# Kernel tuning notes

Hardware: AMD Instinct MI355X
Metric: run time of the kernel (lower is better)

Reference implementation:

```python
import jax, jax.numpy as jnp
import numpy as np

R_FRAC = 0.5  # r_token


def setup_inputs() -> dict:
    key = jax.random.key(0)
    B, T, C = 64, 577, 1024
    hidden_states = jax.random.normal(key, (B, T, C), dtype=jnp.float32)
    return {"hidden_states": hidden_states}


def _match_indices(x, r):
    # Bipartite soft matching (class_token=True, distill_token=False).
    metric = x / jnp.linalg.norm(x, axis=-1, keepdims=True)
    a, b = metric[:, ::2, :], metric[:, 1::2, :]  # [B, Ta, C], [B, Tb, C]
    scores = jnp.einsum('bic,bjc->bij', a, b)     # [B, Ta, Tb]
    scores = scores.at[:, 0, :].set(-jnp.inf)     # protect CLS token (even index 0)
    node_max = scores.max(axis=-1)                # best sim of each src to any dst
    node_idx = scores.argmax(axis=-1)             # matched dst for each src
    edge_idx = jnp.argsort(-node_max, axis=-1)    # descending by similarity
    unm_idx = jnp.sort(edge_idx[:, r:], axis=-1)  # unmerged src (sorted: keeps CLS first)
    src_idx = edge_idx[:, :r]                     # src tokens to merge
    dst_idx = jnp.take_along_axis(node_idx, src_idx, axis=-1)
    return unm_idx, src_idx, dst_idx


def _merge_sum(v, unm_idx, src_idx, dst_idx):
    # Gather unmerged + scatter-add merged src into dst, then concat.
    src, dst = v[:, ::2, :], v[:, 1::2, :]
    unm = jnp.take_along_axis(src, unm_idx[..., None], axis=1)
    srcg = jnp.take_along_axis(src, src_idx[..., None], axis=1)
    dst = jax.vmap(lambda d, i, s: d.at[i].add(s))(dst, dst_idx, srcg)
    return jnp.concatenate([unm, dst], axis=1)


def reference(hidden_states):
    x = hidden_states
    B, T, C = x.shape
    protected = 1  # class token
    r = min(int(R_FRAC * T), (T - protected) // 2)  # 288 for T=577
    unm_idx, src_idx, dst_idx = _match_indices(x, r)
    # merge_wavg with size=None -> size = ones
    size = jnp.ones((B, T, 1), dtype=x.dtype)
    xm = _merge_sum(x * size, unm_idx, src_idx, dst_idx)
    sm = _merge_sum(size, unm_idx, src_idx, dst_idx)
    return xm / sm  # [B, T - r, C]
```

## Files before the change

### kernel.cpp

```cpp
#include <hip/hip_runtime.h>
#include <math.h>


#define B_   64
#define T_   577
#define C_   1024
#define NA   289
#define NB   288
#define EPS_MARGIN 0.01f

#define RPAD 384
#define EXTRA_CAP 12

typedef __bf16 bf16x8 __attribute__((ext_vector_type(8)));
typedef float  floatx4 __attribute__((ext_vector_type(4)));
typedef unsigned long long u64;

#define ECNT_OFF   0
#define GRPWIN_OFF 98304
#define EXTRA_OFF  (GRPWIN_OFF + 1179648)
#define DST_OFF    (EXTRA_OFF + 2359296)

__device__ __forceinline__ u64 shfl_xor_u64(u64 v, int msk) {
  unsigned int lo = (unsigned int)v, hi = (unsigned int)(v >> 32);
  lo = __shfl_xor(lo, msk, 64);
  hi = __shfl_xor(hi, msk, 64);
  return ((u64)hi << 32) | (u64)lo;
}
__device__ __forceinline__ double shfl_xor_f64(double v, int msk) {
  u64 u = __double_as_longlong(v);
  return __longlong_as_double((long long)shfl_xor_u64(u, msk));
}

__device__ __forceinline__ unsigned int fkey(float s) {
  unsigned int fb = __float_as_uint(s);
  return (fb & 0x80000000u) ? ~fb : (fb | 0x80000000u);
}
__device__ __forceinline__ float keyf(unsigned int k) {
  return (k & 0x80000000u) ? __uint_as_float(k ^ 0x80000000u) : __uint_as_float(~k);
}
__device__ __forceinline__ u64 packsc(float s, int col) {
  return ((u64)fkey(s) << 32) | (u64)(0xFFFFFFFFu - (unsigned int)col);
}
__device__ __forceinline__ int pcol(u64 p) {
  return (int)(0xFFFFFFFFu - (unsigned int)(p & 0xFFFFFFFFull));
}
__device__ __forceinline__ float pscore(u64 p) { return keyf((unsigned int)(p >> 32)); }

__device__ __forceinline__ unsigned int pk_bf16_trunc(unsigned int e1, unsigned int e0) {
  return __builtin_amdgcn_perm(e1, e0, 0x07060302u);
}

__device__ __forceinline__ void load16f(const float* x, size_t off, float* v) {
  const float4* p = (const float4*)(x + off);
  float4 a = p[0], b = p[1], c = p[2], d = p[3];
  v[0]=a.x; v[1]=a.y; v[2]=a.z; v[3]=a.w;
  v[4]=b.x; v[5]=b.y; v[6]=b.z; v[7]=b.w;
  v[8]=c.x; v[9]=c.y; v[10]=c.z; v[11]=c.w;
  v[12]=d.x; v[13]=d.y; v[14]=d.z; v[15]=d.w;
}

__global__ __launch_bounds__(256) void k_prep(const float* __restrict__ x,
                                              unsigned int* __restrict__ y) {
  int wv = threadIdx.x >> 6, lane = threadIdx.x & 63;
  int token = blockIdx.x * 4 + wv;
  int t = token % T_;
  int r8 = (t >> 1) & 7;

  float v[16];
  load16f(x, (size_t)token * C_ + lane * 16, v);
  float ss = 0.f;
#pragma unroll
  for (int i = 0; i < 16; ++i) ss += v[i] * v[i];
#pragma unroll
  for (int d = 1; d < 64; d <<= 1) ss += __shfl_xor(ss, d, 64);
  float rn = rsqrtf(ss);
#pragma unroll
  for (int i = 0; i < 16; ++i) v[i] *= rn;

  uint4 g0, g1;
  g0.x = pk_bf16_trunc(__float_as_uint(v[1]),  __float_as_uint(v[0]));
  g0.y = pk_bf16_trunc(__float_as_uint(v[3]),  __float_as_uint(v[2]));
  g0.z = pk_bf16_trunc(__float_as_uint(v[5]),  __float_as_uint(v[4]));
  g0.w = pk_bf16_trunc(__float_as_uint(v[7]),  __float_as_uint(v[6]));
  g1.x = pk_bf16_trunc(__float_as_uint(v[9]),  __float_as_uint(v[8]));
  g1.y = pk_bf16_trunc(__float_as_uint(v[11]), __float_as_uint(v[10]));
  g1.z = pk_bf16_trunc(__float_as_uint(v[13]), __float_as_uint(v[12]));
  g1.w = pk_bf16_trunc(__float_as_uint(v[15]), __float_as_uint(v[14]));

  int ga = 2 * lane, gb = 2 * lane + 1;
  int da = (ga & ~7) | ((ga & 7) ^ r8);
  int db = (gb & ~7) | ((gb & 7) ^ r8);
  uint4* yb = (uint4*)((char*)y + (size_t)token * 2048);
  yb[da] = g0;
  yb[db] = g1;
}


#define GLOADLDS16(GP, LP)                                                    \
  __builtin_amdgcn_global_load_lds(                                           \
      (const __attribute__((address_space(1))) void*)(GP),                    \
      (__attribute__((address_space(3))) void*)(LP), 16, 0, 0)

#define STAGE(CUR, KC) do {                                                   \
  _Pragma("unroll")                                                           \
  for (int e_ = 0; e_ < 6; ++e_)                                              \
    GLOADLDS16(src[e_] + (KC) * 128, smem[CUR] + ldsoff[e_]);                 \
} while (0)

#define MFMAC(BUFP) do {                                                      \
  const unsigned char* buf_ = (BUFP);                                         \
  _Pragma("unroll")                                                           \
  for (int s_ = 0; s_ < 2; ++s_) {                                            \
    int slot_ = (s_ * 4 + q) ^ sw;                                            \
    bf16x8 af_[3], bg_[3];                                                    \
    _Pragma("unroll")                                                         \
    for (int ii_ = 0; ii_ < 3; ++ii_)                                         \
      af_[ii_] = *(const bf16x8*)(buf_ + ((ib + ii_) * 16 + m) * 128 + slot_ * 16); \
    _Pragma("unroll")                                                         \
    for (int jj_ = 0; jj_ < 3; ++jj_)                                         \
      bg_[jj_] = *(const bf16x8*)(buf_ + 12288 + ((jb + jj_) * 16 + m) * 128 + slot_ * 16); \
    _Pragma("unroll")                                                         \
    for (int ii_ = 0; ii_ < 3; ++ii_)                                         \
      _Pragma("unroll")                                                       \
      for (int jj_ = 0; jj_ < 3; ++jj_)                                       \
        acc[ii_][jj_] = __builtin_amdgcn_mfma_f32_16x16x32_bf16(af_[ii_], bg_[jj_], acc[ii_][jj_], 0, 0, 0); \
  }                                                                           \
} while (0)

__global__ __launch_bounds__(256, 2) void k_scores(const unsigned int* __restrict__ y,
                                                   u64* __restrict__ grpwin,
                                                   unsigned int* __restrict__ ecnt,
                                                   u64* __restrict__ extras) {
  __shared__ unsigned char smem[2][24576];
  int tid = threadIdx.x;
  int b  = blockIdx.x;
  int rt = blockIdx.y;
  int ct = blockIdx.z;
  int wv = tid >> 6, lane = tid & 63;
  int m = lane & 15, q = lane >> 4;
  int sw = m & 7;

  const char* src[6];
  int ldsoff[6];
#pragma unroll
  for (int e = 0; e < 6; ++e) {
    int L = ((wv * 6 + e) * 64 + lane) * 16;
    int row = L >> 7;
    int sl  = (L >> 4) & 7;
    int isB = row >= 96;
    int r2  = isB ? row - 96 : row;
    int tok;
    if (isB) tok = 2 * (ct * 96 + r2) + 1;
    else { tok = 2 * (rt * 96 + r2); if (tok > 576) tok = 576; }
    src[e] = (const char*)y + (size_t)(b * T_ + tok) * 2048 + sl * 16;
    ldsoff[e] = (wv * 6 + e) * 1024;
  }

  floatx4 acc[3][3];
#pragma unroll
  for (int ii = 0; ii < 3; ++ii)
#pragma unroll
    for (int jj = 0; jj < 3; ++jj) acc[ii][jj] = (floatx4){0, 0, 0, 0};

  const int ib = (wv >> 1) * 3;
  const int jb = (wv & 1) * 3;

  STAGE(0, 0);
  __syncthreads();
  int cur = 0;
  for (int kc = 0; kc < 15; ++kc) {
    STAGE(cur ^ 1, kc + 1);
    MFMAC(smem[cur]);
    __syncthreads();
    cur ^= 1;
  }
  MFMAC(smem[cur]);

  int g = ct * 2 + (wv & 1);
#pragma unroll
  for (int ii = 0; ii < 3; ++ii) {
#pragma unroll
    for (int r = 0; r < 4; ++r) {
      u64 pj[3];
#pragma unroll
      for (int jj = 0; jj < 3; ++jj) {
        float s = acc[ii][jj][r];
        pj[jj] = packsc(s, ct * 96 + (jb + jj) * 16 + m);
      }
      u64 pk = pj[0];
      if (pj[1] > pk) pk = pj[1];
      if (pj[2] > pk) pk = pj[2];
#pragma unroll
      for (int d = 1; d < 16; d <<= 1) {
        u64 o = shfl_xor_u64(pk, d);
        if (o > pk) pk = o;
      }
      int grow = rt * 96 + (ib + ii) * 16 + q * 4 + r;
      float thr = pscore(pk) - EPS_MARGIN;
      size_t rbase = (size_t)b * RPAD + grow;
#pragma unroll
      for (int jj = 0; jj < 3; ++jj) {
        if (pj[jj] != pk && pscore(pj[jj]) >= thr) {
          unsigned int idx = atomicAdd(&ecnt[rbase], 1u);
          if (idx < EXTRA_CAP) extras[rbase * EXTRA_CAP + idx] = pj[jj];
        }
      }
      if (m == 0) grpwin[rbase * 6 + g] = pk;
    }
  }
}

__global__ __launch_bounds__(256) void k_recheck(const float* __restrict__ x,
                                                 const u64* __restrict__ grpwin,
                                                 const unsigned int* __restrict__ ecnt,
                                                 const u64* __restrict__ extras,
                                                 int* __restrict__ dst) {
  int wid = threadIdx.x >> 6, lane = threadIdx.x & 63;
  int gw = blockIdx.x * 4 + wid;
  int b = gw / NB, i = gw - b * NB + 1;
  size_t rbase = (size_t)b * RPAD + i;

  u64 v = (lane < 6) ? grpwin[rbase * 6 + lane] : 0ull;
#pragma unroll
  for (int d = 1; d < 8; d <<= 1) {
    u64 o = shfl_xor_u64(v, d);
    if (o > v) v = o;
  }
  {
    unsigned int lo = (unsigned int)v, hi = (unsigned int)(v >> 32);
    lo = __shfl(lo, 0, 64); hi = __shfl(hi, 0, 64);
    v = ((u64)hi << 32) | lo;
  }
  float thr = pscore(v) - EPS_MARGIN;

  u64 cand[14]; int nc = 0;
#pragma unroll
  for (int t = 0; t < 6; ++t) {
    u64 w = grpwin[rbase * 6 + t];
    if (pscore(w) >= thr && nc < 14) cand[nc++] = w;
  }
  unsigned int ec = ecnt[rbase]; if (ec > EXTRA_CAP) ec = EXTRA_CAP;
  for (unsigned int t = 0; t < ec; ++t) {
    u64 w = extras[rbase * EXTRA_CAP + t];
    if (pscore(w) >= thr && nc < 14) cand[nc++] = w;
  }

  int best;
  if (nc <= 1) {
    best = pcol(v);
  } else {
    float av[16];
    load16f(x, (size_t)(b * T_ + 2 * i) * C_ + lane * 16, av);
    double bs = -1e300; int bc = 1 << 30;
    for (int c = 0; c < nc; ++c) {
      int col = pcol(cand[c]);
      float bv[16];
      load16f(x, (size_t)(b * T_ + 2 * col + 1) * C_ + lane * 16, bv);
      double dot = 0.0, nsq = 0.0;
#pragma unroll
      for (int t = 0; t < 16; ++t) {
        dot += (double)av[t] * (double)bv[t];
        nsq += (double)bv[t] * (double)bv[t];
      }
#pragma unroll
      for (int d = 32; d >= 1; d >>= 1) {
        dot += shfl_xor_f64(dot, d);
        nsq += shfl_xor_f64(nsq, d);
      }
      double s = dot / sqrt(nsq);
      if (s > bs || (s == bs && col < bc)) { bs = s; bc = col; }
    }
    best = bc;
  }
  if (lane == 0) dst[b * NA + i] = best;
}

__global__ __launch_bounds__(256) void k_merge(const float* __restrict__ x,
                                               const int* __restrict__ dst,
                                               float* __restrict__ out) {
  __shared__ int dstv[NA];
  __shared__ unsigned short lists[4][292];
  __shared__ int cnts[4];
  int b = blockIdx.y, tid = threadIdx.x;
  int orow_base = blockIdx.x * 4;

  for (int i = tid; i < NA; i += 256) dstv[i] = (i >= 1) ? dst[b * NA + i] : -1;
  if (tid < 4) cnts[tid] = 0;
  __syncthreads();

  for (int i = 1 + tid; i <= 288; i += 256) {
    int d = dstv[i];
#pragma unroll
    for (int w4 = 0; w4 < 4; ++w4) {
      int orow_w = orow_base + w4;
      if (orow_w >= 1 && orow_w < NA && d == orow_w - 1) {
        int idx = atomicAdd(&cnts[w4], 1);
        lists[w4][idx] = (unsigned short)i;
      }
    }
  }
  __syncthreads();

  int wv = tid >> 6, lane = tid & 63;
  int orow = orow_base + wv;
  if (orow >= NA) return;

  const size_t xb = (size_t)b * T_ * C_;
  int c0 = lane * 16;
  float acc[16];
  float inv = 1.0f;

  if (orow == 0) {
    load16f(x, xb + c0, acc);
  } else {
    int j = orow - 1;
    load16f(x, xb + (size_t)(2 * j + 1) * C_ + c0, acc);
    int cnt = cnts[wv];
    for (int e = 0; e < cnt; ++e) {
      int i = lists[wv][e];
      float tv[16];
      load16f(x, xb + (size_t)(2 * i) * C_ + c0, tv);
#pragma unroll
      for (int t = 0; t < 16; ++t) acc[t] += tv[t];
    }
    inv = 1.0f / (float)(cnt + 1);
  }

  float4* op = (float4*)(out + ((size_t)b * NA + orow) * C_ + c0);
  op[0] = make_float4(acc[0]*inv,  acc[1]*inv,  acc[2]*inv,  acc[3]*inv);
  op[1] = make_float4(acc[4]*inv,  acc[5]*inv,  acc[6]*inv,  acc[7]*inv);
  op[2] = make_float4(acc[8]*inv,  acc[9]*inv,  acc[10]*inv, acc[11]*inv);
  op[3] = make_float4(acc[12]*inv, acc[13]*inv, acc[14]*inv, acc[15]*inv);
}

extern "C" void kernel_launch(void* const* d_in, const int* in_sizes, int n_in,
                              void* d_out, int out_size, void* d_ws, size_t ws_size,
                              hipStream_t stream) {
  const float* x = (const float*)d_in[0];
  float* out     = (float*)d_out;
  char* ws = (char*)d_ws;
  unsigned int* ecnt = (unsigned int*)(ws + ECNT_OFF);
  u64* grpwin        = (u64*)(ws + GRPWIN_OFF);
  u64* extras        = (u64*)(ws + EXTRA_OFF);
  int* dst           = (int*)(ws + DST_OFF);

  unsigned int* y = (unsigned int*)d_out;

  hipMemsetAsync(ecnt, 0, (size_t)B_ * RPAD * sizeof(unsigned int), stream);
  k_prep   <<<(B_ * T_) / 4, 256, 0, stream>>>(x, y);
  k_scores <<<dim3(B_, 4, 3), 256, 0, stream>>>(y, grpwin, ecnt, extras);
  k_recheck<<<B_ * NB / 4, 256, 0, stream>>>(x, grpwin, ecnt, extras, dst);
  k_merge  <<<dim3((NA + 3) / 4, B_), 256, 0, stream>>>(x, dst, out);
}
```

Measured before the change: 345.5 us.

## Fuse score GEMM, argmax and recheck into one per-row-tile kernel

The separate scores and recheck kernels, the memset and the global workspace for group winners and extras are replaced by one kernel. Each block computes a 32-row by 288-column score tile in LDS, takes the row max with a wave reduction, and rechecks near-ties in fp64 against the original fp32 inputs. This removes two launches, a memset and global round-trips of candidate data. In exchange, A rows are staged per 32-row tile while the full B set is reloaded by each of the 9 row tiles. The tie margin is also tightened, so fewer rows fall into the slow fp64 recheck path.

```diff
diff --git a/kernel.cpp b/kernel.cpp
--- a/kernel.cpp
+++ b/kernel.cpp
@@ -7,19 +7,13 @@
 #define C_   1024
 #define NA   289
 #define NB   288
-#define EPS_MARGIN 0.01f
-
-#define RPAD 384
-#define EXTRA_CAP 12
+#define EPS_MARGIN 0.0025f
 
 typedef __bf16 bf16x8 __attribute__((ext_vector_type(8)));
 typedef float  floatx4 __attribute__((ext_vector_type(4)));
 typedef unsigned long long u64;
 
-#define ECNT_OFF   0
-#define GRPWIN_OFF 98304
-#define EXTRA_OFF  (GRPWIN_OFF + 1179648)
-#define DST_OFF    (EXTRA_OFF + 2359296)
+#define DST_OFF 0
 
 __device__ __forceinline__ u64 shfl_xor_u64(u64 v, int msk) {
   unsigned int lo = (unsigned int)v, hi = (unsigned int)(v >> 32);
@@ -59,6 +53,11 @@
   v[8]=c.x; v[9]=c.y; v[10]=c.z; v[11]=c.w;
   v[12]=d.x; v[13]=d.y; v[14]=d.z; v[15]=d.w;
 }
+
+#define GLOADLDS16(GP, LP)                                                    \
+  __builtin_amdgcn_global_load_lds(                                           \
+      (const __attribute__((address_space(1))) void*)(GP),                    \
+      (__attribute__((address_space(3))) void*)(LP), 16, 0, 0)
 
 __global__ __launch_bounds__(256) void k_prep(const float* __restrict__ x,
                                               unsigned int* __restrict__ y) {
@@ -97,183 +96,157 @@
 }
 
 
-#define GLOADLDS16(GP, LP)                                                    \
-  __builtin_amdgcn_global_load_lds(                                           \
-      (const __attribute__((address_space(1))) void*)(GP),                    \
-      (__attribute__((address_space(3))) void*)(LP), 16, 0, 0)
-
-#define STAGE(CUR, KC) do {                                                   \
+#define STAGE2(CUR, KC) do {                                                  \
   _Pragma("unroll")                                                           \
-  for (int e_ = 0; e_ < 6; ++e_)                                              \
+  for (int e_ = 0; e_ < 10; ++e_)                                             \
     GLOADLDS16(src[e_] + (KC) * 128, smem[CUR] + ldsoff[e_]);                 \
 } while (0)
 
-#define MFMAC(BUFP) do {                                                      \
+#define MFMAC2(BUFP) do {                                                     \
   const unsigned char* buf_ = (BUFP);                                         \
   _Pragma("unroll")                                                           \
   for (int s_ = 0; s_ < 2; ++s_) {                                            \
     int slot_ = (s_ * 4 + q) ^ sw;                                            \
-    bf16x8 af_[3], bg_[3];                                                    \
+    bf16x8 af_, bg_[9];                                                       \
+    af_ = *(const bf16x8*)(buf_ + (rfrag * 16 + m) * 128 + slot_ * 16);       \
     _Pragma("unroll")                                                         \
-    for (int ii_ = 0; ii_ < 3; ++ii_)                                         \
-      af_[ii_] = *(const bf16x8*)(buf_ + ((ib + ii_) * 16 + m) * 128 + slot_ * 16); \
+    for (int jj_ = 0; jj_ < 9; ++jj_)                                         \
+      bg_[jj_] = *(const bf16x8*)(buf_ + 4096 + ((cbase + jj_ * 16) + m) * 128 + slot_ * 16); \
     _Pragma("unroll")                                                         \
-    for (int jj_ = 0; jj_ < 3; ++jj_)                                         \
-      bg_[jj_] = *(const bf16x8*)(buf_ + 12288 + ((jb + jj_) * 16 + m) * 128 + slot_ * 16); \
-    _Pragma("unroll")                                                         \
-    for (int ii_ = 0; ii_ < 3; ++ii_)                                         \
-      _Pragma("unroll")                                                       \
-      for (int jj_ = 0; jj_ < 3; ++jj_)                                       \
-        acc[ii_][jj_] = __builtin_amdgcn_mfma_f32_16x16x32_bf16(af_[ii_], bg_[jj_], acc[ii_][jj_], 0, 0, 0); \
+    for (int jj_ = 0; jj_ < 9; ++jj_)                                         \
+      acc[jj_] = __builtin_amdgcn_mfma_f32_16x16x32_bf16(af_, bg_[jj_], acc[jj_], 0, 0, 0); \
   }                                                                           \
 } while (0)
 
-__global__ __launch_bounds__(256, 2) void k_scores(const unsigned int* __restrict__ y,
-                                                   u64* __restrict__ grpwin,
-                                                   unsigned int* __restrict__ ecnt,
-                                                   u64* __restrict__ extras) {
-  __shared__ unsigned char smem[2][24576];
+__global__ __launch_bounds__(256, 2) void k_spick(const unsigned int* __restrict__ y,
+                                                  const float* __restrict__ x,
+                                                  int* __restrict__ dst) {
+  __shared__ unsigned char smem[2][40960];
   int tid = threadIdx.x;
   int b  = blockIdx.x;
   int rt = blockIdx.y;
-  int ct = blockIdx.z;
   int wv = tid >> 6, lane = tid & 63;
   int m = lane & 15, q = lane >> 4;
   int sw = m & 7;
 
-  const char* src[6];
-  int ldsoff[6];
-#pragma unroll
-  for (int e = 0; e < 6; ++e) {
-    int L = ((wv * 6 + e) * 64 + lane) * 16;
+  const char* src[10];
+  int ldsoff[10];
+#pragma unroll
+  for (int e = 0; e < 10; ++e) {
+    int u = wv * 10 + e;
+    int L = u * 1024 + lane * 16;
     int row = L >> 7;
-    int sl  = (L >> 4) & 7;
-    int isB = row >= 96;
-    int r2  = isB ? row - 96 : row;
-    int tok;
-    if (isB) tok = 2 * (ct * 96 + r2) + 1;
-    else { tok = 2 * (rt * 96 + r2); if (tok > 576) tok = 576; }
-    src[e] = (const char*)y + (size_t)(b * T_ + tok) * 2048 + sl * 16;
-    ldsoff[e] = (wv * 6 + e) * 1024;
-  }
-
-  floatx4 acc[3][3];
-#pragma unroll
-  for (int ii = 0; ii < 3; ++ii)
-#pragma unroll
-    for (int jj = 0; jj < 3; ++jj) acc[ii][jj] = (floatx4){0, 0, 0, 0};
-
-  const int ib = (wv >> 1) * 3;
-  const int jb = (wv & 1) * 3;
-
-  STAGE(0, 0);
+    int s  = (L >> 4) & 7;
+    int tok, fslot;
+    if (row < 32) {
+      int l8 = row & 7;
+      int i = rt * 32 + 1 + row;
+      tok = 2 * i;
+      fslot = s ^ l8 ^ ((row + 1) & 7);
+    } else {
+      int j = row - 32;
+      tok = 2 * j + 1;
+      fslot = s;
+    }
+    src[e] = (const char*)y + (size_t)(b * T_ + tok) * 2048 + fslot * 16;
+    ldsoff[e] = u * 1024;
+  }
+
+  floatx4 acc[9];
+#pragma unroll
+  for (int jj = 0; jj < 9; ++jj) acc[jj] = (floatx4){0, 0, 0, 0};
+
+  const int rfrag = wv & 1;
+  const int cbase = (wv >> 1) * 144;
+
+  STAGE2(0, 0);
   __syncthreads();
   int cur = 0;
   for (int kc = 0; kc < 15; ++kc) {
-    STAGE(cur ^ 1, kc + 1);
-    MFMAC(smem[cur]);
+    STAGE2(cur ^ 1, kc + 1);
+    MFMAC2(smem[cur]);
     __syncthreads();
     cur ^= 1;
   }
-  MFMAC(smem[cur]);
-
-  int g = ct * 2 + (wv & 1);
-#pragma unroll
-  for (int ii = 0; ii < 3; ++ii) {
+  MFMAC2(smem[cur]);
+
+  float* sc = (float*)smem[0];
+#pragma unroll
+  for (int jj = 0; jj < 9; ++jj) {
 #pragma unroll
     for (int r = 0; r < 4; ++r) {
-      u64 pj[3];
-#pragma unroll
-      for (int jj = 0; jj < 3; ++jj) {
-        float s = acc[ii][jj][r];
-        pj[jj] = packsc(s, ct * 96 + (jb + jj) * 16 + m);
-      }
-      u64 pk = pj[0];
-      if (pj[1] > pk) pk = pj[1];
-      if (pj[2] > pk) pk = pj[2];
-#pragma unroll
-      for (int d = 1; d < 16; d <<= 1) {
-        u64 o = shfl_xor_u64(pk, d);
-        if (o > pk) pk = o;
-      }
-      int grow = rt * 96 + (ib + ii) * 16 + q * 4 + r;
-      float thr = pscore(pk) - EPS_MARGIN;
-      size_t rbase = (size_t)b * RPAD + grow;
-#pragma unroll
-      for (int jj = 0; jj < 3; ++jj) {
-        if (pj[jj] != pk && pscore(pj[jj]) >= thr) {
-          unsigned int idx = atomicAdd(&ecnt[rbase], 1u);
-          if (idx < EXTRA_CAP) extras[rbase * EXTRA_CAP + idx] = pj[jj];
+      int srow = rfrag * 16 + q * 4 + r;
+      int scol = cbase + jj * 16 + m;
+      sc[srow * 288 + scol] = acc[jj][r];
+    }
+  }
+  __syncthreads();
+
+  for (int rr = 0; rr < 8; ++rr) {
+    int lrow = wv * 8 + rr;
+    int i = rt * 32 + 1 + lrow;
+
+    u64 ps[5]; u64 pk = 0;
+#pragma unroll
+    for (int s5 = 0; s5 < 5; ++s5) {
+      int col = s5 * 64 + lane;
+      ps[s5] = (col < 288) ? packsc(sc[lrow * 288 + col], col) : 0ull;
+      if (ps[s5] > pk) pk = ps[s5];
+    }
+#pragma unroll
+    for (int d = 1; d < 64; d <<= 1) {
+      u64 o = shfl_xor_u64(pk, d);
+      if (o > pk) pk = o;
+    }
+    float thr = pscore(pk) - EPS_MARGIN;
+
+    u64 bal[5]; int nc = 0;
+#pragma unroll
+    for (int s5 = 0; s5 < 5; ++s5) {
+      int col = s5 * 64 + lane;
+      bal[s5] = __ballot(col < 288 && pscore(ps[s5]) >= thr);
+      nc += __popcll(bal[s5]);
+    }
+
+    int best;
+    if (nc <= 1) {
+      best = pcol(pk);
+    } else {
+      int cand[12]; int ncc = 0;
+#pragma unroll
+      for (int s5 = 0; s5 < 5; ++s5) {
+        u64 mask = bal[s5];
+        while (mask && ncc < 12) {
+          int bit = __ffsll((unsigned long long)mask) - 1;
+          mask &= mask - 1;
+          cand[ncc++] = s5 * 64 + bit;
         }
       }
-      if (m == 0) grpwin[rbase * 6 + g] = pk;
-    }
-  }
-}
-
-__global__ __launch_bounds__(256) void k_recheck(const float* __restrict__ x,
-                                                 const u64* __restrict__ grpwin,
-                                                 const unsigned int* __restrict__ ecnt,
-                                                 const u64* __restrict__ extras,
-                                                 int* __restrict__ dst) {
-  int wid = threadIdx.x >> 6, lane = threadIdx.x & 63;
-  int gw = blockIdx.x * 4 + wid;
-  int b = gw / NB, i = gw - b * NB + 1;
-  size_t rbase = (size_t)b * RPAD + i;
-
-  u64 v = (lane < 6) ? grpwin[rbase * 6 + lane] : 0ull;
-#pragma unroll
-  for (int d = 1; d < 8; d <<= 1) {
-    u64 o = shfl_xor_u64(v, d);
-    if (o > v) v = o;
-  }
-  {
-    unsigned int lo = (unsigned int)v, hi = (unsigned int)(v >> 32);
-    lo = __shfl(lo, 0, 64); hi = __shfl(hi, 0, 64);
-    v = ((u64)hi << 32) | lo;
-  }
-  float thr = pscore(v) - EPS_MARGIN;
-
-  u64 cand[14]; int nc = 0;
-#pragma unroll
-  for (int t = 0; t < 6; ++t) {
-    u64 w = grpwin[rbase * 6 + t];
-    if (pscore(w) >= thr && nc < 14) cand[nc++] = w;
-  }
-  unsigned int ec = ecnt[rbase]; if (ec > EXTRA_CAP) ec = EXTRA_CAP;
-  for (unsigned int t = 0; t < ec; ++t) {
-    u64 w = extras[rbase * EXTRA_CAP + t];
-    if (pscore(w) >= thr && nc < 14) cand[nc++] = w;
-  }
-
-  int best;
-  if (nc <= 1) {
-    best = pcol(v);
-  } else {
-    float av[16];
-    load16f(x, (size_t)(b * T_ + 2 * i) * C_ + lane * 16, av);
-    double bs = -1e300; int bc = 1 << 30;
-    for (int c = 0; c < nc; ++c) {
-      int col = pcol(cand[c]);
-      float bv[16];
-      load16f(x, (size_t)(b * T_ + 2 * col + 1) * C_ + lane * 16, bv);
-      double dot = 0.0, nsq = 0.0;
-#pragma unroll
-      for (int t = 0; t < 16; ++t) {
-        dot += (double)av[t] * (double)bv[t];
-        nsq += (double)bv[t] * (double)bv[t];
+      float av[16];
+      load16f(x, (size_t)(b * T_ + 2 * i) * C_ + lane * 16, av);
+      double bs = -1e300; int bc = 1 << 30;
+      for (int c = 0; c < ncc; ++c) {
+        int col = cand[c];
+        float bv[16];
+        load16f(x, (size_t)(b * T_ + 2 * col + 1) * C_ + lane * 16, bv);
+        double dot = 0.0, nsq = 0.0;
+#pragma unroll
+        for (int t = 0; t < 16; ++t) {
+          dot += (double)av[t] * (double)bv[t];
+          nsq += (double)bv[t] * (double)bv[t];
+        }
+#pragma unroll
+        for (int d = 32; d >= 1; d >>= 1) {
+          dot += shfl_xor_f64(dot, d);
+          nsq += shfl_xor_f64(nsq, d);
+        }
+        double s = dot / sqrt(nsq);
+        if (s > bs || (s == bs && col < bc)) { bs = s; bc = col; }
       }
-#pragma unroll
-      for (int d = 32; d >= 1; d >>= 1) {
-        dot += shfl_xor_f64(dot, d);
-        nsq += shfl_xor_f64(nsq, d);
-      }
-      double s = dot / sqrt(nsq);
-      if (s > bs || (s == bs && col < bc)) { bs = s; bc = col; }
-    }
-    best = bc;
-  }
-  if (lane == 0) dst[b * NA + i] = best;
+      best = bc;
+    }
+    if (lane == 0) dst[b * NA + i] = best;
+  }
 }
 
 __global__ __launch_bounds__(256) void k_merge(const float* __restrict__ x,
@@ -308,30 +281,30 @@
 
   const size_t xb = (size_t)b * T_ * C_;
   int c0 = lane * 16;
-  float acc[16];
+  float acc16[16];
   float inv = 1.0f;
 
   if (orow == 0) {
-    load16f(x, xb + c0, acc);
+    load16f(x, xb + c0, acc16);
   } else {
     int j = orow - 1;
-    load16f(x, xb + (size_t)(2 * j + 1) * C_ + c0, acc);
+    load16f(x, xb + (size_t)(2 * j + 1) * C_ + c0, acc16);
     int cnt = cnts[wv];
     for (int e = 0; e < cnt; ++e) {
       int i = lists[wv][e];
       float tv[16];
       load16f(x, xb + (size_t)(2 * i) * C_ + c0, tv);
 #pragma unroll
-      for (int t = 0; t < 16; ++t) acc[t] += tv[t];
+      for (int t = 0; t < 16; ++t) acc16[t] += tv[t];
     }
     inv = 1.0f / (float)(cnt + 1);
   }
 
   float4* op = (float4*)(out + ((size_t)b * NA + orow) * C_ + c0);
-  op[0] = make_float4(acc[0]*inv,  acc[1]*inv,  acc[2]*inv,  acc[3]*inv);
-  op[1] = make_float4(acc[4]*inv,  acc[5]*inv,  acc[6]*inv,  acc[7]*inv);
-  op[2] = make_float4(acc[8]*inv,  acc[9]*inv,  acc[10]*inv, acc[11]*inv);
-  op[3] = make_float4(acc[12]*inv, acc[13]*inv, acc[14]*inv, acc[15]*inv);
+  op[0] = make_float4(acc16[0]*inv,  acc16[1]*inv,  acc16[2]*inv,  acc16[3]*inv);
+  op[1] = make_float4(acc16[4]*inv,  acc16[5]*inv,  acc16[6]*inv,  acc16[7]*inv);
+  op[2] = make_float4(acc16[8]*inv,  acc16[9]*inv,  acc16[10]*inv, acc16[11]*inv);
+  op[3] = make_float4(acc16[12]*inv, acc16[13]*inv, acc16[14]*inv, acc16[15]*inv);
 }
 
 extern "C" void kernel_launch(void* const* d_in, const int* in_sizes, int n_in,
@@ -340,16 +313,11 @@
   const float* x = (const float*)d_in[0];
   float* out     = (float*)d_out;
   char* ws = (char*)d_ws;
-  unsigned int* ecnt = (unsigned int*)(ws + ECNT_OFF);
-  u64* grpwin        = (u64*)(ws + GRPWIN_OFF);
-  u64* extras        = (u64*)(ws + EXTRA_OFF);
-  int* dst           = (int*)(ws + DST_OFF);
+  int* dst = (int*)(ws + DST_OFF);
 
   unsigned int* y = (unsigned int*)d_out;
 
-  hipMemsetAsync(ecnt, 0, (size_t)B_ * RPAD * sizeof(unsigned int), stream);
-  k_prep   <<<(B_ * T_) / 4, 256, 0, stream>>>(x, y);
-  k_scores <<<dim3(B_, 4, 3), 256, 0, stream>>>(y, grpwin, ecnt, extras);
-  k_recheck<<<B_ * NB / 4, 256, 0, stream>>>(x, grpwin, ecnt, extras, dst);
-  k_merge  <<<dim3((NA + 3) / 4, B_), 256, 0, stream>>>(x, dst, out);
-}
+  k_prep <<<(B_ * T_) / 4, 256, 0, stream>>>(x, y);
+  k_spick<<<dim3(B_, 9), 256, 0, stream>>>(y, x, dst);
+  k_merge<<<dim3((NA + 3) / 4, B_), 256, 0, stream>>>(x, dst, out);
+}
```

Result: faster. 315.7 us (-8.6%).
